# Performance work log

Measured on AMD Instinct MI355X. Metric: run time of the kernel, lower is better.

The kernel has to match this reference:

```python
import jax, jax.numpy as jnp
import numpy as np

POOL = 3      # pooling_size
EPS = 0.006   # constant added to each segment mean in the original code


def setup_inputs() -> dict:
    key = jax.random.key(0)
    k1, k2 = jax.random.split(key)
    B, N, D = 8, 3072, 1024          # N divisible by POOL -> no remainder branch
    steps = N // POOL
    x = jax.random.normal(k1, (B, N, D), dtype=jnp.float32)
    # (start, end) shot boundaries, sorted so start <= end, values in [0, N)
    graph = jnp.sort(jax.random.randint(k2, (B, steps, 2), 0, N, dtype=jnp.int64), axis=-1)
    return {"x": x, "graph": graph}


def reference(x, graph):
    B, N, D = x.shape
    steps = N // POOL
    # Exclusive+inclusive prefix sums: c[b, k] = sum over x[b, :k]  -> [B, N+1, D]
    c = jnp.concatenate([jnp.zeros((B, 1, D), x.dtype), jnp.cumsum(x, axis=1)], axis=1)
    s = graph[..., 0]                # [B, steps]
    e = graph[..., 1]                # [B, steps]
    idx_e = jnp.broadcast_to((e + 1)[..., None], (B, steps, D))
    idx_s = jnp.broadcast_to(s[..., None], (B, steps, D))
    seg_sum = jnp.take_along_axis(c, idx_e, axis=1) - jnp.take_along_axis(c, idx_s, axis=1)
    seg_len = (e - s + 1).astype(x.dtype)[..., None]
    seg_mean = seg_sum / seg_len + EPS            # [B, steps, D]
    # fixed-size window mean over consecutive POOL frames
    win_mean = x.reshape(B, steps, POOL, D).mean(axis=2)   # [B, steps, D]
    # original appends (segment mean, window mean) per step -> interleave
    out = jnp.stack([seg_mean, win_mean], axis=2).reshape(B, 2 * steps, D)
    return out
```

## Files before the change

### kernel.cpp

```cpp
#include <hip/hip_runtime.h>


constexpr int Bdim  = 8;
constexpr int Nn    = 3072;
constexpr int Dd    = 1024;
constexpr int STEPS = 1024;
constexpr int CHW   = 4;
constexpr int NCH   = 256;
constexpr int KT    = 8;
constexpr int NKT   = 128;
constexpr int D4    = Dd / 4;
constexpr float EPS = 0.006f;

constexpr size_t WL_E = (size_t)Bdim * STEPS * Dd;
constexpr size_t P_E  = (size_t)Bdim * NCH * Dd;
constexpr size_t O_E  = (size_t)Bdim * (NCH + 1) * Dd;

__device__ __forceinline__ float4 f4add(float4 a, float4 b) {
    return make_float4(a.x + b.x, a.y + b.y, a.z + b.z, a.w + b.w);
}

__global__ __launch_bounds__(256)
void k1_scan(const float4* __restrict__ x4, float4* __restrict__ out4,
             float4* __restrict__ Wl4, float4* __restrict__ P4) {
    const int t  = threadIdx.x;
    const int ch = blockIdx.x;
    const int b  = blockIdx.y;
    const int k0 = ch * CHW;
    const int r0 = k0 * 3;

    const float4* xp = x4   + ((size_t)(b * Nn + r0)) * D4 + t;
    float4*       wl = Wl4  + ((size_t)(b * STEPS + k0)) * D4 + t;
    float4*       op = out4 + ((size_t)b * 2 * STEPS) * D4 + t;

    float4 run = make_float4(0.f, 0.f, 0.f, 0.f);
#pragma unroll
    for (int w = 0; w < CHW; ++w) {
        wl[(size_t)w * D4] = run;
        float4 v0 = xp[(size_t)(3 * w + 0) * D4];
        float4 v1 = xp[(size_t)(3 * w + 1) * D4];
        float4 v2 = xp[(size_t)(3 * w + 2) * D4];
        float4 s3 = f4add(f4add(v0, v1), v2);
        float4 wm = make_float4(s3.x * (1.f / 3.f), s3.y * (1.f / 3.f),
                                s3.z * (1.f / 3.f), s3.w * (1.f / 3.f));
        op[(size_t)(2 * (k0 + w) + 1) * D4] = wm;
        run = f4add(run, s3);
    }
    P4[((size_t)b * NCH + ch) * D4 + t] = run;
}

__global__ __launch_bounds__(128)
void k2_chscan(const float* __restrict__ P, float* __restrict__ O) {
    const int d = blockIdx.x * 128 + threadIdx.x;
    const int b = blockIdx.y;
    const float* p = P + (size_t)b * NCH * Dd + d;
    float*       o = O + (size_t)b * (NCH + 1) * Dd + d;
    float run = 0.f;
#pragma unroll 8
    for (int ch = 0; ch < NCH; ++ch) {
        o[(size_t)ch * Dd] = run;
        run += p[(size_t)ch * Dd];
    }
    o[(size_t)NCH * Dd] = run;
}

__global__ __launch_bounds__(256)
void k3_gather(const float4* __restrict__ x4, const float4* __restrict__ Wl4,
               const float4* __restrict__ O4, const int* __restrict__ graph,
               float4* __restrict__ out4) {
    __shared__ int gbuf[2 * KT];
    const int t  = threadIdx.x;
    const int kt = blockIdx.x;
    const int b  = blockIdx.y;

    const int* gs = graph + ((size_t)(b * STEPS + kt * KT)) * 2;
    if (t < 2 * KT) gbuf[t] = gs[t];
    __syncthreads();

    const float4* xb = x4  + (size_t)b * Nn * D4 + t;
    const float4* wl = Wl4 + (size_t)b * STEPS * D4 + t;
    const float4* oc = O4  + (size_t)b * (NCH + 1) * D4 + t;
    float4*       ob = out4 + (size_t)b * 2 * STEPS * D4 + t;

#pragma unroll
    for (int j = 0; j < KT; ++j) {
        int s = gbuf[2 * j];
        int e = gbuf[2 * j + 1];

        int m1 = s / 3, r1 = s - 3 * m1;
        float4 cs = f4add(oc[(size_t)(m1 >> 2) * D4], wl[(size_t)m1 * D4]);
        if (r1 > 0) cs = f4add(cs, xb[(size_t)(3 * m1) * D4]);
        if (r1 > 1) cs = f4add(cs, xb[(size_t)(3 * m1 + 1) * D4]);

        int ie = e + 1;
        float4 ce;
        if (ie == Nn) {
            ce = oc[(size_t)NCH * D4];
        } else {
            int m2 = ie / 3, r2 = ie - 3 * m2;
            ce = f4add(oc[(size_t)(m2 >> 2) * D4], wl[(size_t)m2 * D4]);
            if (r2 > 0) ce = f4add(ce, xb[(size_t)(3 * m2) * D4]);
            if (r2 > 1) ce = f4add(ce, xb[(size_t)(3 * m2 + 1) * D4]);
        }

        float inv = 1.f / (float)(e - s + 1);
        float4 res = make_float4((ce.x - cs.x) * inv + EPS,
                                 (ce.y - cs.y) * inv + EPS,
                                 (ce.z - cs.z) * inv + EPS,
                                 (ce.w - cs.w) * inv + EPS);
        int k = kt * KT + j;
        ob[(size_t)(2 * k) * D4] = res;
    }
}

extern "C" void kernel_launch(void* const* d_in, const int* in_sizes, int n_in,
                              void* d_out, int out_size, void* d_ws, size_t ws_size,
                              hipStream_t stream) {
    const float* x     = (const float*)d_in[0];
    const int*   graph = (const int*)d_in[1];
    float*       out   = (float*)d_out;

    float* Wl = (float*)d_ws;
    float* P  = Wl + WL_E;
    float* O  = P + P_E;

    dim3 g1(NCH, Bdim);
    k1_scan<<<g1, 256, 0, stream>>>((const float4*)x, (float4*)out,
                                    (float4*)Wl, (float4*)P);
    dim3 g2(Dd / 128, Bdim);
    k2_chscan<<<g2, 128, 0, stream>>>(P, O);
    dim3 g3(NKT, Bdim);
    k3_gather<<<g3, 256, 0, stream>>>((const float4*)x, (const float4*)Wl,
                                      (const float4*)O, graph, (float4*)out);
}
```

Before: 220.5 us.

## Parallelize chunk-prefix scan across segments, widen chunks, use nontemporal output stores

Doubles the chunk width in the first scan kernel, halving the number of chunk partials. The chunk-level scan is rewritten from one serial thread per column into a two-level scan: eight segments per column reduce in parallel, combine their totals through shared memory, then write prefixes with float4 accesses. Output stores in the first and third kernels become nontemporal to avoid polluting cache with write-once data. The first kernel now launches half as many blocks, each doing twice the serial work, which reduces its parallelism.

```diff
diff --git a/kernel.cpp b/kernel.cpp
--- a/kernel.cpp
+++ b/kernel.cpp
@@ -5,8 +5,8 @@
 constexpr int Nn    = 3072;
 constexpr int Dd    = 1024;
 constexpr int STEPS = 1024;
-constexpr int CHW   = 4;
-constexpr int NCH   = 256;
+constexpr int CHW   = 8;
+constexpr int NCH   = 128;
 constexpr int KT    = 8;
 constexpr int NKT   = 128;
 constexpr int D4    = Dd / 4;
@@ -14,10 +14,16 @@
 
 constexpr size_t WL_E = (size_t)Bdim * STEPS * Dd;
 constexpr size_t P_E  = (size_t)Bdim * NCH * Dd;
-constexpr size_t O_E  = (size_t)Bdim * (NCH + 1) * Dd;
+
+typedef float nat_f4 __attribute__((ext_vector_type(4)));
 
 __device__ __forceinline__ float4 f4add(float4 a, float4 b) {
     return make_float4(a.x + b.x, a.y + b.y, a.z + b.z, a.w + b.w);
+}
+
+__device__ __forceinline__ void nt_store(float4 v, float4* p) {
+    nat_f4 nv = {v.x, v.y, v.z, v.w};
+    __builtin_nontemporal_store(nv, reinterpret_cast<nat_f4*>(p));
 }
 
 __global__ __launch_bounds__(256)
@@ -43,25 +49,48 @@
         float4 s3 = f4add(f4add(v0, v1), v2);
         float4 wm = make_float4(s3.x * (1.f / 3.f), s3.y * (1.f / 3.f),
                                 s3.z * (1.f / 3.f), s3.w * (1.f / 3.f));
-        op[(size_t)(2 * (k0 + w) + 1) * D4] = wm;
+        nt_store(wm, &op[(size_t)(2 * (k0 + w) + 1) * D4]);
         run = f4add(run, s3);
     }
     P4[((size_t)b * NCH + ch) * D4 + t] = run;
 }
 
-__global__ __launch_bounds__(128)
-void k2_chscan(const float* __restrict__ P, float* __restrict__ O) {
-    const int d = blockIdx.x * 128 + threadIdx.x;
-    const int b = blockIdx.y;
-    const float* p = P + (size_t)b * NCH * Dd + d;
-    float*       o = O + (size_t)b * (NCH + 1) * Dd + d;
-    float run = 0.f;
-#pragma unroll 8
-    for (int ch = 0; ch < NCH; ++ch) {
-        o[(size_t)ch * Dd] = run;
-        run += p[(size_t)ch * Dd];
+__global__ __launch_bounds__(256)
+void k2_chscan(const float4* __restrict__ P4, float4* __restrict__ O4) {
+    __shared__ float4 part[8][33];
+    const int cw  = threadIdx.x & 31;
+    const int seg = threadIdx.x >> 5;
+    const int col = blockIdx.x * 32 + cw;
+    const int b   = blockIdx.y;
+
+    const float4* p = P4 + (size_t)b * NCH * D4 + col;
+    float4 v[16];
+    float4 sum = make_float4(0.f, 0.f, 0.f, 0.f);
+#pragma unroll
+    for (int i = 0; i < 16; ++i) {
+        v[i] = p[(size_t)(seg * 16 + i) * D4];
+        sum = f4add(sum, v[i]);
     }
-    o[(size_t)NCH * Dd] = run;
+    part[seg][cw] = sum;
+    __syncthreads();
+    if (threadIdx.x < 32) {
+        float4 run = make_float4(0.f, 0.f, 0.f, 0.f);
+#pragma unroll
+        for (int s = 0; s < 8; ++s) {
+            float4 t2 = part[s][threadIdx.x];
+            part[s][threadIdx.x] = run;
+            run = f4add(run, t2);
+        }
+    }
+    __syncthreads();
+    float4 run = part[seg][cw];
+    float4* o = O4 + (size_t)b * (NCH + 1) * D4 + col;
+#pragma unroll
+    for (int i = 0; i < 16; ++i) {
+        o[(size_t)(seg * 16 + i) * D4] = run;
+        run = f4add(run, v[i]);
+    }
+    if (seg == 7) o[(size_t)NCH * D4] = run;
 }
 
 __global__ __launch_bounds__(256)
@@ -88,7 +117,7 @@
         int e = gbuf[2 * j + 1];
 
         int m1 = s / 3, r1 = s - 3 * m1;
-        float4 cs = f4add(oc[(size_t)(m1 >> 2) * D4], wl[(size_t)m1 * D4]);
+        float4 cs = f4add(oc[(size_t)(m1 >> 3) * D4], wl[(size_t)m1 * D4]);
         if (r1 > 0) cs = f4add(cs, xb[(size_t)(3 * m1) * D4]);
         if (r1 > 1) cs = f4add(cs, xb[(size_t)(3 * m1 + 1) * D4]);
 
@@ -98,7 +127,7 @@
             ce = oc[(size_t)NCH * D4];
         } else {
             int m2 = ie / 3, r2 = ie - 3 * m2;
-            ce = f4add(oc[(size_t)(m2 >> 2) * D4], wl[(size_t)m2 * D4]);
+            ce = f4add(oc[(size_t)(m2 >> 3) * D4], wl[(size_t)m2 * D4]);
             if (r2 > 0) ce = f4add(ce, xb[(size_t)(3 * m2) * D4]);
             if (r2 > 1) ce = f4add(ce, xb[(size_t)(3 * m2 + 1) * D4]);
         }
@@ -109,7 +138,7 @@
                                  (ce.z - cs.z) * inv + EPS,
                                  (ce.w - cs.w) * inv + EPS);
         int k = kt * KT + j;
-        ob[(size_t)(2 * k) * D4] = res;
+        nt_store(res, &ob[(size_t)(2 * k) * D4]);
     }
 }
 
@@ -127,8 +156,8 @@
     dim3 g1(NCH, Bdim);
     k1_scan<<<g1, 256, 0, stream>>>((const float4*)x, (float4*)out,
                                     (float4*)Wl, (float4*)P);
-    dim3 g2(Dd / 128, Bdim);
-    k2_chscan<<<g2, 128, 0, stream>>>(P, O);
+    dim3 g2(D4 / 32, Bdim);
+    k2_chscan<<<g2, 256, 0, stream>>>((const float4*)P, (float4*)O);
     dim3 g3(NKT, Bdim);
     k3_gather<<<g3, 256, 0, stream>>>((const float4*)x, (const float4*)Wl,
                                       (const float4*)O, graph, (float4*)out);
```

Measured after the change: 203.0 us. 1.09x faster.
